# Kernel tuning notes

Measured on AMD Instinct MI355X. Metric: run time of the kernel, lower is better.

## Reference

```python
import jax, jax.numpy as jnp
import numpy as np

N = 50000
E = 625000
D_IN, D_HID, D_EMB, D_OUT = 256, 128, 128, 16


def glorot(key, shape):
    lim = jnp.sqrt(6.0 / (shape[0] + shape[1]))
    return jax.random.uniform(key, shape, jnp.float32, -lim, lim)


def setup_inputs() -> dict:
    key = jax.random.key(0)
    ks = jax.random.split(key, 8)
    x = jax.random.normal(ks[0], (N, D_IN), jnp.float32)
    edge_index = jax.random.randint(ks[1], (2, E), 0, N, jnp.int64)
    edge_weight = jax.random.uniform(ks[2], (E,), jnp.float32)
    return {
        "x": x,
        "edge_weight": edge_weight,
        "W1": glorot(ks[3], (D_IN, D_HID)),
        "b1": jnp.zeros((D_HID,), jnp.float32),
        "W2": glorot(ks[4], (D_HID, D_HID)),
        "b2": jnp.zeros((D_HID,), jnp.float32),
        "W3": glorot(ks[5], (D_HID, D_EMB)),
        "b3": jnp.zeros((D_EMB,), jnp.float32),
        "fc_w": glorot(ks[6], (D_EMB, D_OUT)),
        "fc_b": jnp.zeros((D_OUT,), jnp.float32),
        "edge_index": edge_index,
    }


def digcn_conv(x, edge_index, norm, W, b):
    # dense transform, then edge-weighted gather/scatter-add (SpMM)
    h = x @ W                                  # [N, d_out]
    msg = h[edge_index[0]] * norm[:, None]     # [E, d_out]
    agg = jax.ops.segment_sum(msg, edge_index[1], num_segments=N)
    return agg + b


def reference(x, edge_weight, W1, b1, W2, b2, W3, b3, fc_w, fc_b, edge_index):
    # eval mode: dropout is identity
    h = jax.nn.relu(digcn_conv(x, edge_index, edge_weight, W1, b1))
    h = jax.nn.relu(digcn_conv(h, edge_index, edge_weight, W2, b2))
    emb = digcn_conv(h, edge_index, edge_weight, W3, b3)
    y = emb @ fc_w + fc_b
    return emb, jax.nn.log_softmax(y, axis=1)
```

## Files before the change

### kernel.cpp

```cpp
#include <hip/hip_runtime.h>

#define D_IN 256
#define D_HID 128
#define NPB 512
#define BCAP 8192

typedef __bf16 bf16;
typedef bf16 bf16x8 __attribute__((ext_vector_type(8)));
typedef float f32x4 __attribute__((ext_vector_type(4)));
typedef const __attribute__((address_space(1))) unsigned gu32;
typedef __attribute__((address_space(3))) unsigned lu32;

__global__ void k_prep(const float* __restrict__ W1, const float* __restrict__ W2,
                       const float* __restrict__ W3, const float* __restrict__ fcw,
                       bf16* __restrict__ B1, bf16* __restrict__ B2,
                       bf16* __restrict__ B3, float* __restrict__ fcwT,
                       int* __restrict__ gcnt, int ncnt) {
  int idx = blockIdx.x * blockDim.x + threadIdx.x;
  {
    const float* W; bf16* B; int r;
    if (idx < 32768)      { W = W1; B = B1; r = idx; }
    else if (idx < 49152) { W = W2; B = B2; r = idx - 32768; }
    else                  { W = W3; B = B3; r = idx - 49152; }
    int e = r & 7, l = (r >> 3) & 63, f = r >> 9;
    int ct = f & 7, kt = f >> 3;
    int k = kt * 32 + ((l >> 4) << 3) + e;
    int c = ct * 16 + (l & 15);
    B[r] = (bf16)W[k * 128 + c];
  }
  if (idx < 2048) {
    int c = idx >> 7, k = idx & 127;
    fcwT[idx] = fcw[k * 16 + c];
  }
  if (idx < ncnt) gcnt[idx] = 0;
}

__global__ __launch_bounds__(256) void k_bin(const int* __restrict__ src,
                                             const int* __restrict__ dst,
                                             const float* __restrict__ ew, int E,
                                             int* __restrict__ gcnt,
                                             int2* __restrict__ bins) {
  __shared__ int lcnt[128], lbase[128], lcur[128], gbase[128];
  __shared__ int stot;
  __shared__ int2 stage[2048];
  const int t = threadIdx.x;
  const int e0 = blockIdx.x * 2048;

  if (t < 128) lcnt[t] = 0;
  __syncthreads();

  int2 ent[8]; int bk[8];
  #pragma unroll
  for (int i = 0; i < 8; ++i) {
    int e = e0 + i * 256 + t;
    bool v = e < E;
    int d = v ? dst[e] : 0;
    int s = v ? src[e] : 0;
    float w = v ? ew[e] : 0.f;
    int b = d >> 9;
    bk[i] = v ? b : -1;
    ent[i] = make_int2(s | ((d & 511) << 16) | (b << 25), __float_as_int(w));
    if (v) atomicAdd(&lcnt[b], 1);
  }
  __syncthreads();

  int v = (t < 128) ? lcnt[t] : 0;
  if (t < 128) lbase[t] = v;
  __syncthreads();
  for (int off = 1; off < 128; off <<= 1) {
    int u = (t < 128 && t >= off) ? lbase[t - off] : 0;
    __syncthreads();
    if (t < 128) lbase[t] += u;
    __syncthreads();
  }
  if (t == 127) stot = lbase[127];
  if (t < 128) {
    int ex = lbase[t] - v;
    lbase[t] = ex;
    lcur[t] = ex;
    gbase[t] = (v > 0) ? atomicAdd(&gcnt[t * 16], v) : 0;
  }
  __syncthreads();

  #pragma unroll
  for (int i = 0; i < 8; ++i) {
    if (bk[i] >= 0) {
      int pos = atomicAdd(&lcur[bk[i]], 1);
      stage[pos] = ent[i];
    }
  }
  __syncthreads();

  const int tot = stot;
  for (int j = t; j < tot; j += 256) {
    int2 en = stage[j];
    int b = (en.x >> 25) & 0x7F;
    int gp = gbase[b] + (j - lbase[b]);
    if (gp < BCAP)
      bins[(size_t)b * BCAP + gp] = make_int2(en.x & 0x01FFFFFF, en.y);
  }
}

__global__ __launch_bounds__(128) void k_bsum(const int* __restrict__ gcnt, int nbk,
                                              int* __restrict__ rbase,
                                              int* __restrict__ rptr, int N) {
  __shared__ int sm[128];
  int t = threadIdx.x;
  int v = (t < nbk) ? min(gcnt[t * 16], BCAP) : 0;
  sm[t] = v; __syncthreads();
  for (int off = 1; off < 128; off <<= 1) {
    int u = (t >= off) ? sm[t - off] : 0;
    __syncthreads();
    sm[t] += u; __syncthreads();
  }
  if (t < nbk) rbase[t] = sm[t] - v;
  if (t == 127) rptr[N] = sm[127];
}

__global__ __launch_bounds__(512) void k_build(const int2* __restrict__ bins,
                                               const int* __restrict__ gcnt,
                                               const int* __restrict__ rbase,
                                               int* __restrict__ rptr,
                                               int2* __restrict__ esw, int N) {
  __shared__ int deg[512], sm[512], cur[512];
  __shared__ int cnt, base;
  const int b = blockIdx.x, t = threadIdx.x;
  const int n0 = b << 9;
  deg[t] = 0;
  if (t == 0) { cnt = min(gcnt[b * 16], BCAP); base = rbase[b]; }
  __syncthreads();
  const int2* bp = bins + (size_t)b * BCAP;
  const int c = cnt;
  for (int i = t; i < c; i += 512) atomicAdd(&deg[(bp[i].x >> 16) & 511], 1);
  __syncthreads();
  sm[t] = deg[t];
  __syncthreads();
  for (int off = 1; off < 512; off <<= 1) {
    int u = (t >= off) ? sm[t - off] : 0;
    __syncthreads();
    sm[t] += u;
    __syncthreads();
  }
  int ex = sm[t] - deg[t];
  cur[t] = ex;
  if (n0 + t < N) rptr[n0 + t] = base + ex;
  __syncthreads();
  for (int i = t; i < c; i += 512) {
    int2 en = bp[i];
    int pos = atomicAdd(&cur[(en.x >> 16) & 511], 1);
    esw[base + pos] = make_int2(en.x & 0xFFFF, en.y);
  }
}

template<int K, bool A_IS_F32>
__global__ __launch_bounds__(256) void k_gemm5(const void* __restrict__ Ain,
                                               const bf16* __restrict__ Bp,
                                               bf16* __restrict__ Hb, int N) {
  constexpr int NKT = K / 32;
  constexpr int NST = (K * 128) / (256 * 8);
  __shared__ bf16 Bs[K * 128];
  const int t = threadIdx.x;
  const int wave = t >> 6;
  const int lane = t & 63;
  const int l16 = lane & 15;
  const int g = lane >> 4;
  const int row0 = blockIdx.x * 64 + wave * 16;
  const int arow = row0 + l16;
  const int arow_c = (arow < N) ? arow : (N - 1);

  #pragma unroll
  for (int i = 0; i < NST; ++i) {
    const bf16* gsrc = Bp + (size_t)(i * 256 + t) * 8;
    bf16* ldst = Bs + (size_t)(i * 256 + (t & ~63)) * 8;
    __builtin_amdgcn_global_load_lds((gu32*)gsrc, (lu32*)ldst, 16, 0, 0);
  }

  bf16x8 afr[NKT];
  if constexpr (A_IS_F32) {
    const float* Af = (const float*)Ain + (size_t)arow_c * K + g * 8;
    f32x4 f0[NKT], f1[NKT];
    #pragma unroll
    for (int kt = 0; kt < NKT; ++kt) {
      f0[kt] = *reinterpret_cast<const f32x4*>(Af + kt * 32);
      f1[kt] = *reinterpret_cast<const f32x4*>(Af + kt * 32 + 4);
    }
    #pragma unroll
    for (int kt = 0; kt < NKT; ++kt) {
      bf16x8 a;
      a[0] = (bf16)f0[kt][0]; a[1] = (bf16)f0[kt][1];
      a[2] = (bf16)f0[kt][2]; a[3] = (bf16)f0[kt][3];
      a[4] = (bf16)f1[kt][0]; a[5] = (bf16)f1[kt][1];
      a[6] = (bf16)f1[kt][2]; a[7] = (bf16)f1[kt][3];
      afr[kt] = a;
    }
  } else {
    const bf16* Ab = (const bf16*)Ain + (size_t)arow_c * K + g * 8;
    #pragma unroll
    for (int kt = 0; kt < NKT; ++kt)
      afr[kt] = *reinterpret_cast<const bf16x8*>(Ab + kt * 32);
  }

  __syncthreads();

  f32x4 acc[8];
  #pragma unroll
  for (int ct = 0; ct < 8; ++ct) acc[ct] = f32x4{0.f, 0.f, 0.f, 0.f};

  #pragma unroll
  for (int kt = 0; kt < NKT; ++kt) {
    #pragma unroll
    for (int ct = 0; ct < 8; ++ct) {
      bf16x8 b = *reinterpret_cast<const bf16x8*>(Bs + (kt * 8 + ct) * 512 + lane * 8);
      acc[ct] = __builtin_amdgcn_mfma_f32_16x16x32_bf16(afr[kt], b, acc[ct], 0, 0, 0);
    }
  }

  const int orow = row0 + 4 * g;
  #pragma unroll
  for (int ct = 0; ct < 8; ++ct) {
    #pragma unroll
    for (int r = 0; r < 4; ++r) {
      if (orow + r < N)
        Hb[(size_t)(orow + r) * 128 + ct * 16 + l16] = (bf16)acc[ct][r];
    }
  }
}

template<int MODE>
__global__ __launch_bounds__(256) void k_agg(const bf16* __restrict__ H,
                                             const int* __restrict__ rptr,
                                             const int2* __restrict__ esw,
                                             const float* __restrict__ bias,
                                             void* __restrict__ out, int N) {
  const int wv = threadIdx.x >> 6;
  const int lane = threadIdx.x & 63;
  const int node = blockIdx.x * 8 + wv * 2 + (lane >> 5);
  if (node >= N) return;
  const int l16 = lane & 15;
  const int slot = (lane >> 4) & 1;
  const int p1 = rptr[node + 1];
  float a[8];
  #pragma unroll
  for (int j = 0; j < 8; ++j) a[j] = 0.f;

  int p = rptr[node] + slot;
  for (; p + 2 < p1; p += 4) {
    int2 e0 = esw[p];
    int2 e1 = esw[p + 2];
    bf16x8 h0 = *reinterpret_cast<const bf16x8*>(H + (size_t)e0.x * 128 + l16 * 8);
    bf16x8 h1 = *reinterpret_cast<const bf16x8*>(H + (size_t)e1.x * 128 + l16 * 8);
    float w0 = __int_as_float(e0.y), w1 = __int_as_float(e1.y);
    #pragma unroll
    for (int j = 0; j < 8; ++j)
      a[j] += w0 * (float)h0[j] + w1 * (float)h1[j];
  }
  if (p < p1) {
    int2 e0 = esw[p];
    bf16x8 h0 = *reinterpret_cast<const bf16x8*>(H + (size_t)e0.x * 128 + l16 * 8);
    float w0 = __int_as_float(e0.y);
    #pragma unroll
    for (int j = 0; j < 8; ++j)
      a[j] += w0 * (float)h0[j];
  }
  #pragma unroll
  for (int j = 0; j < 8; ++j) a[j] += __shfl_xor(a[j], 16);

  if ((lane & 16) == 0) {
    float4 b0 = *reinterpret_cast<const float4*>(bias + l16 * 8);
    float4 b1 = *reinterpret_cast<const float4*>(bias + l16 * 8 + 4);
    a[0] += b0.x; a[1] += b0.y; a[2] += b0.z; a[3] += b0.w;
    a[4] += b1.x; a[5] += b1.y; a[6] += b1.z; a[7] += b1.w;
    if (MODE == 0) {
      bf16x8 o;
      #pragma unroll
      for (int j = 0; j < 8; ++j) o[j] = (bf16)fmaxf(a[j], 0.f);
      *reinterpret_cast<bf16x8*>((bf16*)out + (size_t)node * 128 + l16 * 8) = o;
    } else {
      f32x4 o0 = {a[0], a[1], a[2], a[3]};
      f32x4 o1 = {a[4], a[5], a[6], a[7]};
      float* op = (float*)out + (size_t)node * 128 + l16 * 8;
      *reinterpret_cast<f32x4*>(op) = o0;
      *reinterpret_cast<f32x4*>(op + 4) = o1;
    }
  }
}

__global__ __launch_bounds__(256) void k_fc_lsm(const float* __restrict__ emb,
                                                const float* __restrict__ fcwT,
                                                const float* __restrict__ fcb,
                                                float* __restrict__ out, int N) {
  __shared__ float wl[16 * 128];
  __shared__ float fb[16];
  const int t = threadIdx.x;
  {
    const float4* s4 = reinterpret_cast<const float4*>(fcwT);
    float4* d4 = reinterpret_cast<float4*>(wl);
    d4[t] = s4[t];
    d4[t + 256] = s4[t + 256];
  }
  if (t < 16) fb[t] = fcb[t];
  __syncthreads();

  const int node = blockIdx.x * 256 + t;
  if (node >= N) return;
  const float4* er = reinterpret_cast<const float4*>(emb + (size_t)node * 128);

  float acc[16];
  #pragma unroll
  for (int c = 0; c < 16; ++c) acc[c] = fb[c];

  #pragma unroll 4
  for (int k4 = 0; k4 < 32; ++k4) {
    float4 e = er[k4];
    #pragma unroll
    for (int c = 0; c < 16; ++c) {
      float4 w = reinterpret_cast<const float4*>(wl + c * 128)[k4];
      acc[c] += e.x * w.x + e.y * w.y + e.z * w.z + e.w * w.w;
    }
  }

  float m = acc[0];
  #pragma unroll
  for (int c = 1; c < 16; ++c) m = fmaxf(m, acc[c]);
  float s = 0.f;
  #pragma unroll
  for (int c = 0; c < 16; ++c) s += __expf(acc[c] - m);
  float lse = m + __logf(s);
  float* op = out + (size_t)node * 16;
  #pragma unroll
  for (int c4 = 0; c4 < 4; ++c4) {
    f32x4 o = {acc[c4 * 4] - lse, acc[c4 * 4 + 1] - lse,
               acc[c4 * 4 + 2] - lse, acc[c4 * 4 + 3] - lse};
    *reinterpret_cast<f32x4*>(op + c4 * 4) = o;
  }
}

extern "C" void kernel_launch(void* const* d_in, const int* in_sizes, int n_in,
                              void* d_out, int out_size, void* d_ws, size_t ws_size,
                              hipStream_t stream) {
  const float* x   = (const float*)d_in[0];
  const float* ew  = (const float*)d_in[1];
  const float* W1  = (const float*)d_in[2];
  const float* b1  = (const float*)d_in[3];
  const float* W2  = (const float*)d_in[4];
  const float* b2  = (const float*)d_in[5];
  const float* W3  = (const float*)d_in[6];
  const float* b3  = (const float*)d_in[7];
  const float* fcw = (const float*)d_in[8];
  const float* fcb = (const float*)d_in[9];
  const int*   ei  = (const int*)d_in[10];

  const int N = in_sizes[0] / D_IN;
  const int E = in_sizes[1];
  const int* srcI = ei;
  const int* dstI = ei + E;
  const int NBK = (N + NPB - 1) / NPB;
  const int ncnt = NBK * 16;

  char* ws = (char*)d_ws;
  size_t o = 0;
  auto take = [&](size_t b) -> char* {
    char* p = ws + o;
    o += (b + 255) & ~(size_t)255;
    return p;
  };
  bf16*  hb0  = (bf16*)take((size_t)N * 128 * 2);
  bf16*  hb1  = (bf16*)take((size_t)N * 128 * 2);
  bf16*  Bp1  = (bf16*)take((size_t)D_IN * 128 * 2);
  bf16*  Bp2  = (bf16*)take((size_t)D_HID * 128 * 2);
  bf16*  Bp3  = (bf16*)take((size_t)D_HID * 128 * 2);
  float* fcwT = (float*)take((size_t)2048 * 4);
  int*   rptr = (int*)take((size_t)(N + 1) * 4);
  int*   gcnt = (int*)take((size_t)ncnt * 4);
  int*   rbase= (int*)take((size_t)NBK * 4);
  int2*  bins = (int2*)take((size_t)NBK * BCAP * 8);
  int2*  esw  = (int2*)take((size_t)E * 8);
  (void)ws_size; (void)n_in; (void)out_size;

  k_prep<<<256, 256, 0, stream>>>(W1, W2, W3, fcw, Bp1, Bp2, Bp3, fcwT, gcnt, ncnt);

  int bb = (E + 2047) / 2048;
  k_bin<<<bb, 256, 0, stream>>>(srcI, dstI, ew, E, gcnt, bins);
  k_bsum<<<1, 128, 0, stream>>>(gcnt, NBK, rbase, rptr, N);
  k_build<<<NBK, 512, 0, stream>>>(bins, gcnt, rbase, rptr, esw, N);

  float* emb = (float*)d_out;
  float* lsm = emb + (size_t)N * 128;
  int gb5 = (N + 63) / 64;
  int ab = (N + 7) / 8;

  k_gemm5<D_IN, true><<<gb5, 256, 0, stream>>>(x, Bp1, hb0, N);
  k_agg<0><<<ab, 256, 0, stream>>>(hb0, rptr, esw, b1, hb1, N);
  k_gemm5<D_HID, false><<<gb5, 256, 0, stream>>>(hb1, Bp2, hb0, N);
  k_agg<0><<<ab, 256, 0, stream>>>(hb0, rptr, esw, b2, hb1, N);
  k_gemm5<D_HID, false><<<gb5, 256, 0, stream>>>(hb1, Bp3, hb0, N);
  k_agg<1><<<ab, 256, 0, stream>>>(hb0, rptr, esw, b3, emb, N);
  k_fc_lsm<<<(N + 255) / 256, 256, 0, stream>>>(emb, fcwT, fcb, lsm, N);
}
```

Baseline: 175.2 us.

## Fuse aggregation with following dense transform in layers 1-2

Adds a kernel that aggregates neighbor features for 64 nodes into shared memory, applies bias and ReLU, then multiplies by the next layer's weight with MFMA in the same block. It replaces two agg+gemm kernel pairs, removing the intermediate H write and read and two launches. In exchange each block holds a 32KB weight tile plus a 16KB tile in LDS, which lowers occupancy, and the gather phase runs fewer concurrent nodes per block with a barrier before the GEMM.

```diff
diff --git a/kernel.cpp b/kernel.cpp
--- a/kernel.cpp
+++ b/kernel.cpp
@@ -222,6 +222,106 @@
     for (int r = 0; r < 4; ++r) {
       if (orow + r < N)
         Hb[(size_t)(orow + r) * 128 + ct * 16 + l16] = (bf16)acc[ct][r];
+    }
+  }
+}
+
+__global__ __launch_bounds__(256) void k_fuse(const bf16* __restrict__ G,
+                                              const int* __restrict__ rptr,
+                                              const int2* __restrict__ esw,
+                                              const float* __restrict__ bias,
+                                              const bf16* __restrict__ Bp,
+                                              bf16* __restrict__ Out, int N) {
+  __shared__ bf16 Ws[128 * 128];
+  __shared__ bf16 Hs[64 * 128];
+  const int t = threadIdx.x;
+  const int wave = t >> 6;
+  const int lane = t & 63;
+  const int l16 = lane & 15;
+  const int g = lane >> 4;
+  const int slot = (lane >> 4) & 1;
+  const int half = lane >> 5;
+  const int base = blockIdx.x * 64;
+
+  #pragma unroll
+  for (int i = 0; i < 8; ++i) {
+    const bf16* gsrc = Bp + (size_t)(i * 256 + t) * 8;
+    bf16* ldst = Ws + (size_t)(i * 256 + (t & ~63)) * 8;
+    __builtin_amdgcn_global_load_lds((gu32*)gsrc, (lu32*)ldst, 16, 0, 0);
+  }
+
+  for (int rnd = 0; rnd < 8; ++rnd) {
+    const int r = rnd * 8 + wave * 2 + half;
+    const int node = base + r;
+    const bool valid = node < N;
+    const int nc = valid ? node : 0;
+    const int p1 = valid ? rptr[nc + 1] : 0;
+    int p = valid ? rptr[nc] + slot : 0;
+    float a[8];
+    #pragma unroll
+    for (int j = 0; j < 8; ++j) a[j] = 0.f;
+    for (; p + 2 < p1; p += 4) {
+      int2 e0 = esw[p];
+      int2 e1 = esw[p + 2];
+      bf16x8 h0 = *reinterpret_cast<const bf16x8*>(G + (size_t)e0.x * 128 + l16 * 8);
+      bf16x8 h1 = *reinterpret_cast<const bf16x8*>(G + (size_t)e1.x * 128 + l16 * 8);
+      float w0 = __int_as_float(e0.y), w1 = __int_as_float(e1.y);
+      #pragma unroll
+      for (int j = 0; j < 8; ++j)
+        a[j] += w0 * (float)h0[j] + w1 * (float)h1[j];
+    }
+    if (p < p1) {
+      int2 e0 = esw[p];
+      bf16x8 h0 = *reinterpret_cast<const bf16x8*>(G + (size_t)e0.x * 128 + l16 * 8);
+      float w0 = __int_as_float(e0.y);
+      #pragma unroll
+      for (int j = 0; j < 8; ++j)
+        a[j] += w0 * (float)h0[j];
+    }
+    #pragma unroll
+    for (int j = 0; j < 8; ++j) a[j] += __shfl_xor(a[j], 16);
+    if ((lane & 16) == 0) {
+      float4 b0 = *reinterpret_cast<const float4*>(bias + l16 * 8);
+      float4 b1 = *reinterpret_cast<const float4*>(bias + l16 * 8 + 4);
+      bf16x8 o;
+      o[0] = (bf16)fmaxf(a[0] + b0.x, 0.f); o[1] = (bf16)fmaxf(a[1] + b0.y, 0.f);
+      o[2] = (bf16)fmaxf(a[2] + b0.z, 0.f); o[3] = (bf16)fmaxf(a[3] + b0.w, 0.f);
+      o[4] = (bf16)fmaxf(a[4] + b1.x, 0.f); o[5] = (bf16)fmaxf(a[5] + b1.y, 0.f);
+      o[6] = (bf16)fmaxf(a[6] + b1.z, 0.f); o[7] = (bf16)fmaxf(a[7] + b1.w, 0.f);
+      int sidx = r * 128 + ((l16 * 8) ^ ((r & 7) << 3));
+      *reinterpret_cast<bf16x8*>(Hs + sidx) = o;
+    }
+  }
+  __syncthreads();
+
+  const int arow_l = wave * 16 + l16;
+  bf16x8 afr[4];
+  #pragma unroll
+  for (int kt = 0; kt < 4; ++kt) {
+    int e0 = kt * 32 + g * 8;
+    afr[kt] = *reinterpret_cast<const bf16x8*>(
+        Hs + arow_l * 128 + (e0 ^ ((arow_l & 7) << 3)));
+  }
+
+  f32x4 acc[8];
+  #pragma unroll
+  for (int ct = 0; ct < 8; ++ct) acc[ct] = f32x4{0.f, 0.f, 0.f, 0.f};
+  #pragma unroll
+  for (int kt = 0; kt < 4; ++kt) {
+    #pragma unroll
+    for (int ct = 0; ct < 8; ++ct) {
+      bf16x8 b = *reinterpret_cast<const bf16x8*>(Ws + (kt * 8 + ct) * 512 + lane * 8);
+      acc[ct] = __builtin_amdgcn_mfma_f32_16x16x32_bf16(afr[kt], b, acc[ct], 0, 0, 0);
+    }
+  }
+
+  const int orow = base + wave * 16 + 4 * g;
+  #pragma unroll
+  for (int ct = 0; ct < 8; ++ct) {
+    #pragma unroll
+    for (int r = 0; r < 4; ++r) {
+      if (orow + r < N)
+        Out[(size_t)(orow + r) * 128 + ct * 16 + l16] = (bf16)acc[ct][r];
     }
   }
 }
@@ -386,14 +486,12 @@
 
   float* emb = (float*)d_out;
   float* lsm = emb + (size_t)N * 128;
-  int gb5 = (N + 63) / 64;
+  int gb = (N + 63) / 64;
   int ab = (N + 7) / 8;
 
-  k_gemm5<D_IN, true><<<gb5, 256, 0, stream>>>(x, Bp1, hb0, N);
-  k_agg<0><<<ab, 256, 0, stream>>>(hb0, rptr, esw, b1, hb1, N);
-  k_gemm5<D_HID, false><<<gb5, 256, 0, stream>>>(hb1, Bp2, hb0, N);
-  k_agg<0><<<ab, 256, 0, stream>>>(hb0, rptr, esw, b2, hb1, N);
-  k_gemm5<D_HID, false><<<gb5, 256, 0, stream>>>(hb1, Bp3, hb0, N);
+  k_gemm5<D_IN, true><<<gb, 256, 0, stream>>>(x, Bp1, hb0, N);
+  k_fuse<<<gb, 256, 0, stream>>>(hb0, rptr, esw, b1, Bp2, hb1, N);
+  k_fuse<<<gb, 256, 0, stream>>>(hb1, rptr, esw, b2, Bp3, hb0, N);
   k_agg<1><<<ab, 256, 0, stream>>>(hb0, rptr, esw, b3, emb, N);
   k_fc_lsm<<<(N + 255) / 256, 256, 0, stream>>>(emb, fcwT, fcb, lsm, N);
 }
```

After: 230.9 us. +31.7%, slower.

## Merge edge binning and first-layer GEMM into one heterogeneous launch

Applied to the files above, without the earlier changes.

Edge binning and the first dense transform (x @ W1) are independent, so they are merged into a single kernel whose blocks split by block index: the first BB blocks bin edges and the rest compute the GEMM. This lets the memory-bound binning overlap with the MFMA GEMM and removes one kernel launch boundary. The cost is that the shared memory footprint becomes a 64 KB union for all blocks, which may lower occupancy for the binning blocks, and k_gemm5 is trimmed to the bf16-input path only.

```diff
diff --git a/kernel.cpp b/kernel.cpp
--- a/kernel.cpp
+++ b/kernel.cpp
@@ -35,69 +35,137 @@
   if (idx < ncnt) gcnt[idx] = 0;
 }
 
-__global__ __launch_bounds__(256) void k_bin(const int* __restrict__ src,
-                                             const int* __restrict__ dst,
-                                             const float* __restrict__ ew, int E,
-                                             int* __restrict__ gcnt,
-                                             int2* __restrict__ bins) {
-  __shared__ int lcnt[128], lbase[128], lcur[128], gbase[128];
-  __shared__ int stot;
-  __shared__ int2 stage[2048];
+__global__ __launch_bounds__(256) void k_bin_gemm1(
+    const int* __restrict__ src, const int* __restrict__ dst,
+    const float* __restrict__ ew, int E, int* __restrict__ gcnt,
+    int2* __restrict__ bins, int BB,
+    const float* __restrict__ x, const bf16* __restrict__ Bp,
+    bf16* __restrict__ Hb, int N) {
+  __shared__ __align__(16) char smraw[65536];
   const int t = threadIdx.x;
-  const int e0 = blockIdx.x * 2048;
-
-  if (t < 128) lcnt[t] = 0;
-  __syncthreads();
-
-  int2 ent[8]; int bk[8];
-  #pragma unroll
-  for (int i = 0; i < 8; ++i) {
-    int e = e0 + i * 256 + t;
-    bool v = e < E;
-    int d = v ? dst[e] : 0;
-    int s = v ? src[e] : 0;
-    float w = v ? ew[e] : 0.f;
-    int b = d >> 9;
-    bk[i] = v ? b : -1;
-    ent[i] = make_int2(s | ((d & 511) << 16) | (b << 25), __float_as_int(w));
-    if (v) atomicAdd(&lcnt[b], 1);
-  }
-  __syncthreads();
-
-  int v = (t < 128) ? lcnt[t] : 0;
-  if (t < 128) lbase[t] = v;
-  __syncthreads();
-  for (int off = 1; off < 128; off <<= 1) {
-    int u = (t < 128 && t >= off) ? lbase[t - off] : 0;
-    __syncthreads();
-    if (t < 128) lbase[t] += u;
-    __syncthreads();
-  }
-  if (t == 127) stot = lbase[127];
-  if (t < 128) {
-    int ex = lbase[t] - v;
-    lbase[t] = ex;
-    lcur[t] = ex;
-    gbase[t] = (v > 0) ? atomicAdd(&gcnt[t * 16], v) : 0;
-  }
-  __syncthreads();
-
-  #pragma unroll
-  for (int i = 0; i < 8; ++i) {
-    if (bk[i] >= 0) {
-      int pos = atomicAdd(&lcur[bk[i]], 1);
-      stage[pos] = ent[i];
-    }
-  }
-  __syncthreads();
-
-  const int tot = stot;
-  for (int j = t; j < tot; j += 256) {
-    int2 en = stage[j];
-    int b = (en.x >> 25) & 0x7F;
-    int gp = gbase[b] + (j - lbase[b]);
-    if (gp < BCAP)
-      bins[(size_t)b * BCAP + gp] = make_int2(en.x & 0x01FFFFFF, en.y);
+
+  if (blockIdx.x < BB) {
+    int* lcnt  = (int*)smraw;
+    int* lbase = lcnt + 128;
+    int* lcur  = lcnt + 256;
+    int* gbase = lcnt + 384;
+    int* stotp = lcnt + 512;
+    int2* stage = (int2*)(smraw + 4096);
+    const int e0 = blockIdx.x * 2048;
+
+    if (t < 128) lcnt[t] = 0;
+    __syncthreads();
+
+    int2 ent[8]; int bk[8];
+    #pragma unroll
+    for (int i = 0; i < 8; ++i) {
+      int e = e0 + i * 256 + t;
+      bool v = e < E;
+      int d = v ? dst[e] : 0;
+      int s = v ? src[e] : 0;
+      float w = v ? ew[e] : 0.f;
+      int b = d >> 9;
+      bk[i] = v ? b : -1;
+      ent[i] = make_int2(s | ((d & 511) << 16) | (b << 25), __float_as_int(w));
+      if (v) atomicAdd(&lcnt[b], 1);
+    }
+    __syncthreads();
+
+    int v = (t < 128) ? lcnt[t] : 0;
+    if (t < 128) lbase[t] = v;
+    __syncthreads();
+    for (int off = 1; off < 128; off <<= 1) {
+      int u = (t < 128 && t >= off) ? lbase[t - off] : 0;
+      __syncthreads();
+      if (t < 128) lbase[t] += u;
+      __syncthreads();
+    }
+    if (t == 127) *stotp = lbase[127];
+    if (t < 128) {
+      int ex = lbase[t] - v;
+      lbase[t] = ex;
+      lcur[t] = ex;
+      gbase[t] = (v > 0) ? atomicAdd(&gcnt[t * 16], v) : 0;
+    }
+    __syncthreads();
+
+    #pragma unroll
+    for (int i = 0; i < 8; ++i) {
+      if (bk[i] >= 0) {
+        int pos = atomicAdd(&lcur[bk[i]], 1);
+        stage[pos] = ent[i];
+      }
+    }
+    __syncthreads();
+
+    const int tot = *stotp;
+    for (int j = t; j < tot; j += 256) {
+      int2 en = stage[j];
+      int b = (en.x >> 25) & 0x7F;
+      int gp = gbase[b] + (j - lbase[b]);
+      if (gp < BCAP)
+        bins[(size_t)b * BCAP + gp] = make_int2(en.x & 0x01FFFFFF, en.y);
+    }
+  } else {
+    constexpr int K = 256, NKT = 8, NST = 16;
+    bf16* Bs = (bf16*)smraw;
+    const int wave = t >> 6;
+    const int lane = t & 63;
+    const int l16 = lane & 15;
+    const int g = lane >> 4;
+    const int row0 = (blockIdx.x - BB) * 64 + wave * 16;
+    const int arow = row0 + l16;
+    const int arow_c = (arow < N) ? arow : (N - 1);
+
+    #pragma unroll
+    for (int i = 0; i < NST; ++i) {
+      const bf16* gsrc = Bp + (size_t)(i * 256 + t) * 8;
+      bf16* ldst = Bs + (size_t)(i * 256 + (t & ~63)) * 8;
+      __builtin_amdgcn_global_load_lds((gu32*)gsrc, (lu32*)ldst, 16, 0, 0);
+    }
+
+    bf16x8 afr[NKT];
+    {
+      const float* Af = x + (size_t)arow_c * K + g * 8;
+      f32x4 f0[NKT], f1[NKT];
+      #pragma unroll
+      for (int kt = 0; kt < NKT; ++kt) {
+        f0[kt] = *reinterpret_cast<const f32x4*>(Af + kt * 32);
+        f1[kt] = *reinterpret_cast<const f32x4*>(Af + kt * 32 + 4);
+      }
+      #pragma unroll
+      for (int kt = 0; kt < NKT; ++kt) {
+        bf16x8 a;
+        a[0] = (bf16)f0[kt][0]; a[1] = (bf16)f0[kt][1];
+        a[2] = (bf16)f0[kt][2]; a[3] = (bf16)f0[kt][3];
+        a[4] = (bf16)f1[kt][0]; a[5] = (bf16)f1[kt][1];
+        a[6] = (bf16)f1[kt][2]; a[7] = (bf16)f1[kt][3];
+        afr[kt] = a;
+      }
+    }
+    __syncthreads();
+
+    f32x4 acc[8];
+    #pragma unroll
+    for (int ct = 0; ct < 8; ++ct) acc[ct] = f32x4{0.f, 0.f, 0.f, 0.f};
+    #pragma unroll
+    for (int kt = 0; kt < NKT; ++kt) {
+      #pragma unroll
+      for (int ct = 0; ct < 8; ++ct) {
+        bf16x8 b = *reinterpret_cast<const bf16x8*>(Bs + (kt * 8 + ct) * 512 + lane * 8);
+        acc[ct] = __builtin_amdgcn_mfma_f32_16x16x32_bf16(afr[kt], b, acc[ct], 0, 0, 0);
+      }
+    }
+
+    const int orow = row0 + 4 * g;
+    #pragma unroll
+    for (int ct = 0; ct < 8; ++ct) {
+      #pragma unroll
+      for (int r = 0; r < 4; ++r) {
+        if (orow + r < N)
+          Hb[(size_t)(orow + r) * 128 + ct * 16 + l16] = (bf16)acc[ct][r];
+      }
+    }
   }
 }
 
@@ -152,8 +220,8 @@
   }
 }
 
-template<int K, bool A_IS_F32>
-__global__ __launch_bounds__(256) void k_gemm5(const void* __restrict__ Ain,
+template<int K>
+__global__ __launch_bounds__(256) void k_gemm5(const bf16* __restrict__ Ain,
                                                const bf16* __restrict__ Bp,
                                                bf16* __restrict__ Hb, int N) {
   constexpr int NKT = K / 32;
@@ -176,36 +244,16 @@
   }
 
   bf16x8 afr[NKT];
-  if constexpr (A_IS_F32) {
-    const float* Af = (const float*)Ain + (size_t)arow_c * K + g * 8;
-    f32x4 f0[NKT], f1[NKT];
-    #pragma unroll
-    for (int kt = 0; kt < NKT; ++kt) {
-      f0[kt] = *reinterpret_cast<const f32x4*>(Af + kt * 32);
-      f1[kt] = *reinterpret_cast<const f32x4*>(Af + kt * 32 + 4);
-    }
-    #pragma unroll
-    for (int kt = 0; kt < NKT; ++kt) {
-      bf16x8 a;
-      a[0] = (bf16)f0[kt][0]; a[1] = (bf16)f0[kt][1];
-      a[2] = (bf16)f0[kt][2]; a[3] = (bf16)f0[kt][3];
-      a[4] = (bf16)f1[kt][0]; a[5] = (bf16)f1[kt][1];
-      a[6] = (bf16)f1[kt][2]; a[7] = (bf16)f1[kt][3];
-      afr[kt] = a;
-    }
-  } else {
-    const bf16* Ab = (const bf16*)Ain + (size_t)arow_c * K + g * 8;
-    #pragma unroll
-    for (int kt = 0; kt < NKT; ++kt)
-      afr[kt] = *reinterpret_cast<const bf16x8*>(Ab + kt * 32);
-  }
+  const bf16* Ab = Ain + (size_t)arow_c * K + g * 8;
+  #pragma unroll
+  for (int kt = 0; kt < NKT; ++kt)
+    afr[kt] = *reinterpret_cast<const bf16x8*>(Ab + kt * 32);
 
   __syncthreads();
 
   f32x4 acc[8];
   #pragma unroll
   for (int ct = 0; ct < 8; ++ct) acc[ct] = f32x4{0.f, 0.f, 0.f, 0.f};
-
   #pragma unroll
   for (int kt = 0; kt < NKT; ++kt) {
     #pragma unroll
@@ -380,20 +428,20 @@
   k_prep<<<256, 256, 0, stream>>>(W1, W2, W3, fcw, Bp1, Bp2, Bp3, fcwT, gcnt, ncnt);
 
   int bb = (E + 2047) / 2048;
-  k_bin<<<bb, 256, 0, stream>>>(srcI, dstI, ew, E, gcnt, bins);
+  int gb = (N + 63) / 64;
+  k_bin_gemm1<<<bb + gb, 256, 0, stream>>>(srcI, dstI, ew, E, gcnt, bins, bb,
+                                           x, Bp1, hb0, N);
   k_bsum<<<1, 128, 0, stream>>>(gcnt, NBK, rbase, rptr, N);
   k_build<<<NBK, 512, 0, stream>>>(bins, gcnt, rbase, rptr, esw, N);
 
   float* emb = (float*)d_out;
   float* lsm = emb + (size_t)N * 128;
-  int gb5 = (N + 63) / 64;
   int ab = (N + 7) / 8;
 
-  k_gemm5<D_IN, true><<<gb5, 256, 0, stream>>>(x, Bp1, hb0, N);
   k_agg<0><<<ab, 256, 0, stream>>>(hb0, rptr, esw, b1, hb1, N);
-  k_gemm5<D_HID, false><<<gb5, 256, 0, stream>>>(hb1, Bp2, hb0, N);
+  k_gemm5<D_HID><<<gb, 256, 0, stream>>>(hb1, Bp2, hb0, N);
   k_agg<0><<<ab, 256, 0, stream>>>(hb0, rptr, esw, b2, hb1, N);
-  k_gemm5<D_HID, false><<<gb5, 256, 0, stream>>>(hb1, Bp3, hb0, N);
+  k_gemm5<D_HID><<<gb, 256, 0, stream>>>(hb1, Bp3, hb0, N);
   k_agg<1><<<ab, 256, 0, stream>>>(hb0, rptr, esw, b3, emb, N);
   k_fc_lsm<<<(N + 255) / 256, 256, 0, stream>>>(emb, fcwT, fcb, lsm, N);
 }
```

Result: faster. 169.9 us (-3.0%).
